# Optimization experiments

Hardware: AMD Instinct MI355X
Metric: run time of the kernel (lower is better)

The kernel has to match this reference:

```python
import jax, jax.numpy as jnp
import numpy as np

IRREPS = [0, 1, 2, 3, 4]   # l values; dim = sum(2l+1) = 25
MAX_L = max(IRREPS)
DIM = sum(2 * l + 1 for l in IRREPS)
EPS = 1e-14
N_POINTS = 200000


def _p_terms(i, a, b, l):
    """Ivanic-Ruedenberg P(i,l,a,b) as sparse terms: (coef, flat idx into R1 (3x3), flat idx into D^{l-1})."""
    lp = l - 1
    n = 2 * lp + 1
    row = i + 1  # R1 rows/cols indexed by m in {-1,0,1} -> {0,1,2}
    if b == l:
        return [(1.0, row * 3 + 2, (a + lp) * n + 2 * lp),
                (-1.0, row * 3 + 0, (a + lp) * n + 0)]
    if b == -l:
        return [(1.0, row * 3 + 2, (a + lp) * n + 0),
                (1.0, row * 3 + 0, (a + lp) * n + 2 * lp)]
    return [(1.0, row * 3 + 1, (a + lp) * n + (b + lp))]


def _ru_tables(l):
    """Precompute sparse recurrence tables for building D^l from D^{l-1} and R1."""
    out_idx, rij, ab, coef = [], [], [], []
    n = 2 * l + 1
    for m in range(-l, l + 1):
        for mp in range(-l, l + 1):
            denom = (2 * l) * (2 * l - 1) if abs(mp) == l else (l + mp) * (l - mp)
            d0 = 1.0 if m == 0 else 0.0
            u = np.sqrt((l + m) * (l - m) / denom)
            v = 0.5 * np.sqrt((1 + d0) * (l + abs(m) - 1) * (l + abs(m)) / denom) * (1 - 2 * d0)
            w = -0.5 * np.sqrt(max(l - abs(m) - 1, 0) * (l - abs(m)) / denom) * (1 - d0)
            terms = []
            if u != 0.0:
                terms += [(u * c, i, j) for c, i, j in _p_terms(0, m, mp, l)]
            if v != 0.0:
                if m == 0:
                    terms += [(v * c, i, j) for c, i, j in _p_terms(1, 1, mp, l)]
                    terms += [(v * c, i, j) for c, i, j in _p_terms(-1, -1, mp, l)]
                elif m > 0:
                    s = np.sqrt(2.0) if m == 1 else 1.0
                    terms += [(v * s * c, i, j) for c, i, j in _p_terms(1, m - 1, mp, l)]
                    if m != 1:
                        terms += [(-v * c, i, j) for c, i, j in _p_terms(-1, -m + 1, mp, l)]
                else:
                    if m != -1:
                        terms += [(v * c, i, j) for c, i, j in _p_terms(1, m + 1, mp, l)]
                    s = np.sqrt(2.0) if m == -1 else 1.0
                    terms += [(v * s * c, i, j) for c, i, j in _p_terms(-1, -m - 1, mp, l)]
            if w != 0.0:
                if m > 0:
                    terms += [(w * c, i, j) for c, i, j in _p_terms(1, m + 1, mp, l)]
                    terms += [(w * c, i, j) for c, i, j in _p_terms(-1, -m - 1, mp, l)]
                else:
                    terms += [(w * c, i, j) for c, i, j in _p_terms(1, m - 1, mp, l)]
                    terms += [(-w * c, i, j) for c, i, j in _p_terms(-1, -m + 1, mp, l)]
            o = (m + l) * n + (mp + l)
            for c, i, j in terms:
                out_idx.append(o); rij.append(i); ab.append(j); coef.append(c)
    return (np.asarray(out_idx), np.asarray(rij), np.asarray(ab),
            np.asarray(coef, dtype=np.float32))


_TABLES = {l: _ru_tables(l) for l in range(2, MAX_L + 1)}


def _wigner_blocks(R1, max_l):
    """D^l for real spherical harmonics via Ivanic-Ruedenberg recurrence. R1: (N,3,3)."""
    N = R1.shape[0]
    blocks = {0: jnp.ones((N, 1, 1), R1.dtype), 1: R1}
    r1f = R1.reshape(N, 9)
    for l in range(2, max_l + 1):
        oi, rij, ab, cf = _TABLES[l]
        dprev = blocks[l - 1].reshape(N, (2 * l - 1) ** 2)
        contrib = cf[None, :] * r1f[:, rij] * dprev[:, ab]  # (N, n_terms)
        n = 2 * l + 1
        Dl = jnp.zeros((N, n * n), R1.dtype).at[:, oi].add(contrib)
        blocks[l] = Dl.reshape(N, n, n)
    return blocks


def _forward(xyz):
    # angles of v (normalized=True): theta polar, phi azimuthal
    norm = jnp.linalg.norm(xyz, axis=-1, keepdims=True)
    v = xyz / jnp.maximum(norm, EPS)
    ct = jnp.clip(v[..., 2], -1.0, 1.0)
    theta = jnp.arccos(ct)
    phi = jnp.arctan2(v[..., 1], v[..., 0])
    st, cp, sp = jnp.sin(theta), jnp.cos(phi), jnp.sin(phi)
    z = jnp.zeros_like(ct)
    # R = Ry(-theta) @ Rz(-phi): R @ v = |v| z_hat
    R = jnp.stack([
        jnp.stack([ct * cp, ct * sp, -st], -1),
        jnp.stack([-sp, cp, z], -1),
        jnp.stack([st * cp, st * sp, ct], -1),
    ], -2)  # (N,3,3)
    # real-SH l=1 basis order m=(-1,0,1) <-> (y,z,x)
    p = jnp.array([1, 2, 0])
    R1 = R[:, p][:, :, p]
    blocks = _wigner_blocks(R1, MAX_L)
    N = xyz.shape[0]
    D = jnp.zeros((N, DIM, DIM), xyz.dtype)
    off = 0
    for l in IRREPS:
        d = 2 * l + 1
        D = D.at[:, off:off + d, off:off + d].set(blocks[l])
        off += d
    return D


def setup_inputs() -> dict:
    key = jax.random.key(0)
    xyz = jax.random.normal(key, (N_POINTS, 3), dtype=jnp.float32)
    return {"xyz": xyz}


def reference(xyz):
    return _forward(xyz)
```

## Files before the change

kernel.cpp:

```cpp
#include <hip/hip_runtime.h>
#include <utility>
#include <cstddef>


struct Term { int o; int r; int a; float c; };
struct LTable { int n; Term t[1024]; };

constexpr double csqrt(double x) {
    if (x <= 0.0) return 0.0;
    double g = x < 1.0 ? 1.0 : x;
    for (int i = 0; i < 50; ++i) g = 0.5 * (g + x / g);
    return g;
}
constexpr int cabs_i(int x) { return x < 0 ? -x : x; }
constexpr int cmax_i(int a, int b) { return a > b ? a : b; }

constexpr void add_p(LTable& T, int o, double scale, int i, int a, int b, int l) {
    int lp = l - 1;
    int np = 2 * lp + 1;
    int row = i + 1;
    if (b == l) {
        T.t[T.n++] = Term{o, row * 3 + 2, (a + lp) * np + 2 * lp, (float)scale};
        T.t[T.n++] = Term{o, row * 3 + 0, (a + lp) * np + 0,      (float)(-scale)};
    } else if (b == -l) {
        T.t[T.n++] = Term{o, row * 3 + 2, (a + lp) * np + 0,      (float)scale};
        T.t[T.n++] = Term{o, row * 3 + 0, (a + lp) * np + 2 * lp, (float)scale};
    } else {
        T.t[T.n++] = Term{o, row * 3 + 1, (a + lp) * np + (b + lp), (float)scale};
    }
}

constexpr LTable ru_table(int l) {
    LTable T{};
    int n = 2 * l + 1;
    for (int m = -l; m <= l; ++m) {
        for (int mp = -l; mp <= l; ++mp) {
            double denom = (cabs_i(mp) == l) ? (double)((2 * l) * (2 * l - 1))
                                             : (double)((l + mp) * (l - mp));
            double d0 = (m == 0) ? 1.0 : 0.0;
            double u = csqrt((double)((l + m) * (l - m)) / denom);
            double v = 0.5 * csqrt((1.0 + d0) * (l + cabs_i(m) - 1) * (l + cabs_i(m)) / denom)
                       * (1.0 - 2.0 * d0);
            double w = -0.5 * csqrt((double)cmax_i(l - cabs_i(m) - 1, 0) * (l - cabs_i(m)) / denom)
                       * (1.0 - d0);
            int o = (m + l) * n + (mp + l);
            if (u != 0.0) add_p(T, o, u, 0, m, mp, l);
            if (v != 0.0) {
                if (m == 0) {
                    add_p(T, o, v, 1, 1, mp, l);
                    add_p(T, o, v, -1, -1, mp, l);
                } else if (m > 0) {
                    double s = (m == 1) ? csqrt(2.0) : 1.0;
                    add_p(T, o, v * s, 1, m - 1, mp, l);
                    if (m != 1) add_p(T, o, -v, -1, -m + 1, mp, l);
                } else {
                    if (m != -1) add_p(T, o, v, 1, m + 1, mp, l);
                    double s = (m == -1) ? csqrt(2.0) : 1.0;
                    add_p(T, o, v * s, -1, -m - 1, mp, l);
                }
            }
            if (w != 0.0) {
                if (m > 0) {
                    add_p(T, o, w, 1, m + 1, mp, l);
                    add_p(T, o, w, -1, -m - 1, mp, l);
                } else {
                    add_p(T, o, w, 1, m - 1, mp, l);
                    add_p(T, o, -w, -1, -m + 1, mp, l);
                }
            }
        }
    }
    return T;
}

inline constexpr LTable T2 = ru_table(2);
inline constexpr LTable T3 = ru_table(3);
inline constexpr LTable T4 = ru_table(4);

template<const LTable& T>
constexpr int er_start(int e) {
    for (int i = 0; i < T.n; ++i) if (T.t[i].o == e) return i;
    return 0;
}
template<const LTable& T>
constexpr int er_cnt(int e) {
    int c = 0;
    for (int i = 0; i < T.n; ++i) if (T.t[i].o == e) ++c;
    return c;
}

template<const LTable& T, int S, size_t... K>
__device__ __forceinline__ float sum_terms(const float* __restrict__ R1,
                                           const float* __restrict__ P,
                                           std::index_sequence<K...>) {
    float a = 0.0f;
    ((a = fmaf(T.t[S + (int)K].c, R1[T.t[S + (int)K].r] * P[T.t[S + (int)K].a], a)), ...);
    return a;
}

template<const LTable& T, int l, bool KEEP, int e>
__device__ __forceinline__ void level_one(const float* __restrict__ R1,
                                          const float* __restrict__ P,
                                          float* __restrict__ keep,
                                          float* __restrict__ row) {
    constexpr int S = er_start<T>(e);
    constexpr int C = er_cnt<T>(e);
    float v = sum_terms<T, S>(R1, P, std::make_index_sequence<C>{});
    if constexpr (KEEP) keep[e] = v;
    constexpr int d = 2 * l + 1;
    constexpr int r = e / d, c = e % d;
    constexpr int E625 = (l * l + r) * 25 + (l * l + c);
    row[E625] = v;
}

template<const LTable& T, int l, bool KEEP, size_t... E>
__device__ __forceinline__ void level(const float* __restrict__ R1,
                                      const float* __restrict__ P,
                                      float* __restrict__ keep,
                                      float* __restrict__ row,
                                      std::index_sequence<E...>) {
    (level_one<T, l, KEEP, (int)E>(R1, P, keep, row), ...);
}

template<size_t... E>
__device__ __forceinline__ void write_l1(const float* __restrict__ D1,
                                         float* __restrict__ row,
                                         std::index_sequence<E...>) {
    ((row[(1 + (int)E / 3) * 25 + (1 + (int)E % 3)] = D1[E]), ...);
}

typedef float v4f __attribute__((ext_vector_type(4)));


__global__ __launch_bounds__(256, 2)
void wigner_fused_kernel(const float* __restrict__ xyz, float* __restrict__ out, int Ntot) {
    __shared__ float img[32 * 625];

    const int t = threadIdx.x;
    const int gp = blockIdx.x * 256 + t;

    float x = 0.0f, y = 0.0f, z = 1.0f;
    if (gp < Ntot) {
        x = xyz[3 * gp + 0];
        y = xyz[3 * gp + 1];
        z = xyz[3 * gp + 2];
    }

    const float r2 = x * x + y * y + z * z;
    const float rinv = rsqrtf(fmaxf(r2, 1e-24f));
    const float ct = fminf(fmaxf(z * rinv, -1.0f), 1.0f);
    const float st = sqrtf(fmaxf(1.0f - ct * ct, 0.0f));
    const float rxy2 = x * x + y * y;
    float cp = 1.0f, sp = 0.0f;
    if (rxy2 > 0.0f) {
        const float ri = rsqrtf(rxy2);
        cp = x * ri;
        sp = y * ri;
    }

    v4f* b4 = (v4f*)img;
    const v4f z4 = {0.0f, 0.0f, 0.0f, 0.0f};
#pragma unroll 4
    for (int k = t; k < 5000; k += 256) b4[k] = z4;
    __syncthreads();

    const int p0 = t & 31;
    const long long blk_f = (long long)blockIdx.x * 256 * 625;

    for (int c = 0; c < 8; ++c) {
        const int base_pt = blockIdx.x * 256 + c * 32;
        if (base_pt >= Ntot) break;
        const int vp = min(32, Ntot - base_pt);

        if ((t >> 5) == c && gp < Ntot) {
            float* __restrict__ row = img + p0 * 625;
            row[0] = 1.0f;

            float D1[9] = {cp,      0.0f, -sp,
                           st * sp, ct,   st * cp,
                           ct * sp, -st,  ct * cp};
            write_l1(D1, row, std::make_index_sequence<9>{});

            float D2[25];
            level<T2, 2, true>(D1, D1, D2, row, std::make_index_sequence<25>{});
            float D3[49];
            level<T3, 3, true>(D1, D2, D3, row, std::make_index_sequence<49>{});
            level<T4, 4, false>(D1, D3, nullptr, row, std::make_index_sequence<81>{});
        }
        __syncthreads();

        const long long out_f = blk_f + (long long)c * 32 * 625;
        if (vp == 32) {
            const v4f* src = (const v4f*)img;
            v4f* dst = (v4f*)(out + out_f);
#pragma unroll 4
            for (int k = t; k < 5000; k += 256) {
                __builtin_nontemporal_store(src[k], dst + k);
            }
        } else {
            const int vf = vp * 625;
            for (int k = t; k < vf; k += 256) {
                out[out_f + k] = img[k];
            }
        }
        __syncthreads();
    }
}

extern "C" void kernel_launch(void* const* d_in, const int* in_sizes, int n_in,
                              void* d_out, int out_size, void* d_ws, size_t ws_size,
                              hipStream_t stream) {
    const float* xyz = (const float*)d_in[0];
    float* out = (float*)d_out;
    const int N = in_sizes[0] / 3;
    const int blocks = (N + 255) / 256;
    hipLaunchKernelGGL(wigner_fused_kernel, dim3(blocks), dim3(256), 0, stream,
                       xyz, out, N);
}
```

Before: 538.7 us.

## Split per-point Wigner recurrence across all eight warps via shared-memory levels

```diff
diff --git a/kernel.cpp b/kernel.cpp
--- a/kernel.cpp
+++ b/kernel.cpp
@@ -89,42 +89,61 @@
     return c;
 }
 
-template<const LTable& T, int S, size_t... K>
-__device__ __forceinline__ float sum_terms(const float* __restrict__ R1,
-                                           const float* __restrict__ P,
+constexpr int poff(int a, int l) {
+    int lp = l - 1;
+    int n = 2 * lp + 1;
+    int rr = a / n, cc = a % n;
+    return (lp * lp + rr) * 25 + (lp * lp + cc);
+}
+
+template<const LTable& T, int S, bool PREG, int l, int K>
+__device__ __forceinline__ float term_val(const float* R1, const float* P) {
+    constexpr Term tm = T.t[S + K];
+    constexpr int idx = PREG ? tm.a : poff(tm.a, l);
+    return R1[tm.r] * P[idx];
+}
+
+template<const LTable& T, int S, bool PREG, int l, size_t... K>
+__device__ __forceinline__ float sum_terms(const float* R1, const float* P,
                                            std::index_sequence<K...>) {
     float a = 0.0f;
-    ((a = fmaf(T.t[S + (int)K].c, R1[T.t[S + (int)K].r] * P[T.t[S + (int)K].a], a)), ...);
+    ((a = fmaf(T.t[S + (int)K].c, term_val<T, S, PREG, l, (int)K>(R1, P), a)), ...);
     return a;
 }
 
-template<const LTable& T, int l, bool KEEP, int e>
-__device__ __forceinline__ void level_one(const float* __restrict__ R1,
-                                          const float* __restrict__ P,
-                                          float* __restrict__ keep,
-                                          float* __restrict__ row) {
+template<const LTable& T, int l, bool PREG, int e>
+__device__ __forceinline__ void entry_one(const float* R1, const float* P,
+                                          float* row) {
     constexpr int S = er_start<T>(e);
     constexpr int C = er_cnt<T>(e);
-    float v = sum_terms<T, S>(R1, P, std::make_index_sequence<C>{});
-    if constexpr (KEEP) keep[e] = v;
+    float v = sum_terms<T, S, PREG, l>(R1, P, std::make_index_sequence<C>{});
     constexpr int d = 2 * l + 1;
-    constexpr int r = e / d, c = e % d;
-    constexpr int E625 = (l * l + r) * 25 + (l * l + c);
-    row[E625] = v;
-}
-
-template<const LTable& T, int l, bool KEEP, size_t... E>
-__device__ __forceinline__ void level(const float* __restrict__ R1,
-                                      const float* __restrict__ P,
-                                      float* __restrict__ keep,
-                                      float* __restrict__ row,
-                                      std::index_sequence<E...>) {
-    (level_one<T, l, KEEP, (int)E>(R1, P, keep, row), ...);
+    constexpr int off = (l * l + e / d) * 25 + (l * l + e % d);
+    row[off] = v;
+}
+
+template<const LTable& T, int l, bool PREG, int G, size_t... K>
+__device__ __forceinline__ void group_entries(const float* R1, const float* P,
+                                              float* row, std::index_sequence<K...>) {
+    (entry_one<T, l, PREG, G + 8 * (int)K>(R1, P, row), ...);
+}
+
+template<const LTable& T, int l, bool PREG>
+__device__ __forceinline__ void group_dispatch(int g, const float* R1,
+                                               const float* P, float* row) {
+    constexpr int NE = (2 * l + 1) * (2 * l + 1);
+    if      (g == 0) group_entries<T, l, PREG, 0>(R1, P, row, std::make_index_sequence<(NE - 0 + 7) / 8>{});
+    else if (g == 1) group_entries<T, l, PREG, 1>(R1, P, row, std::make_index_sequence<(NE - 1 + 7) / 8>{});
+    else if (g == 2) group_entries<T, l, PREG, 2>(R1, P, row, std::make_index_sequence<(NE - 2 + 7) / 8>{});
+    else if (g == 3) group_entries<T, l, PREG, 3>(R1, P, row, std::make_index_sequence<(NE - 3 + 7) / 8>{});
+    else if (g == 4) group_entries<T, l, PREG, 4>(R1, P, row, std::make_index_sequence<(NE - 4 + 7) / 8>{});
+    else if (g == 5) group_entries<T, l, PREG, 5>(R1, P, row, std::make_index_sequence<(NE - 5 + 7) / 8>{});
+    else if (g == 6) group_entries<T, l, PREG, 6>(R1, P, row, std::make_index_sequence<(NE - 6 + 7) / 8>{});
+    else             group_entries<T, l, PREG, 7>(R1, P, row, std::make_index_sequence<(NE - 7 + 7) / 8>{});
 }
 
 template<size_t... E>
-__device__ __forceinline__ void write_l1(const float* __restrict__ D1,
-                                         float* __restrict__ row,
+__device__ __forceinline__ void write_l1(const float* D1, float* row,
                                          std::index_sequence<E...>) {
     ((row[(1 + (int)E / 3) * 25 + (1 + (int)E % 3)] = D1[E]), ...);
 }
@@ -137,26 +156,8 @@
     __shared__ float img[32 * 625];
 
     const int t = threadIdx.x;
-    const int gp = blockIdx.x * 256 + t;
-
-    float x = 0.0f, y = 0.0f, z = 1.0f;
-    if (gp < Ntot) {
-        x = xyz[3 * gp + 0];
-        y = xyz[3 * gp + 1];
-        z = xyz[3 * gp + 2];
-    }
-
-    const float r2 = x * x + y * y + z * z;
-    const float rinv = rsqrtf(fmaxf(r2, 1e-24f));
-    const float ct = fminf(fmaxf(z * rinv, -1.0f), 1.0f);
-    const float st = sqrtf(fmaxf(1.0f - ct * ct, 0.0f));
-    const float rxy2 = x * x + y * y;
-    float cp = 1.0f, sp = 0.0f;
-    if (rxy2 > 0.0f) {
-        const float ri = rsqrtf(rxy2);
-        cp = x * ri;
-        sp = y * ri;
-    }
+    const int p = t & 31;
+    const int g = t >> 5;
 
     v4f* b4 = (v4f*)img;
     const v4f z4 = {0.0f, 0.0f, 0.0f, 0.0f};
@@ -164,29 +165,51 @@
     for (int k = t; k < 5000; k += 256) b4[k] = z4;
     __syncthreads();
 
-    const int p0 = t & 31;
     const long long blk_f = (long long)blockIdx.x * 256 * 625;
+    float* row = img + p * 625;
 
     for (int c = 0; c < 8; ++c) {
         const int base_pt = blockIdx.x * 256 + c * 32;
         if (base_pt >= Ntot) break;
         const int vp = min(32, Ntot - base_pt);
-
-        if ((t >> 5) == c && gp < Ntot) {
-            float* __restrict__ row = img + p0 * 625;
-            row[0] = 1.0f;
-
-            float D1[9] = {cp,      0.0f, -sp,
-                           st * sp, ct,   st * cp,
-                           ct * sp, -st,  ct * cp};
-            write_l1(D1, row, std::make_index_sequence<9>{});
-
-            float D2[25];
-            level<T2, 2, true>(D1, D1, D2, row, std::make_index_sequence<25>{});
-            float D3[49];
-            level<T3, 3, true>(D1, D2, D3, row, std::make_index_sequence<49>{});
-            level<T4, 4, false>(D1, D3, nullptr, row, std::make_index_sequence<81>{});
-        }
+        const int pt = base_pt + p;
+        const bool live = (p < vp);
+
+        float x = 0.0f, y = 0.0f, z = 1.0f;
+        if (live) {
+            x = xyz[3 * pt + 0];
+            y = xyz[3 * pt + 1];
+            z = xyz[3 * pt + 2];
+        }
+        const float r2 = x * x + y * y + z * z;
+        const float rinv = rsqrtf(fmaxf(r2, 1e-24f));
+        const float ct = fminf(fmaxf(z * rinv, -1.0f), 1.0f);
+        const float st = sqrtf(fmaxf(1.0f - ct * ct, 0.0f));
+        const float rxy2 = x * x + y * y;
+        float cp = 1.0f, sp = 0.0f;
+        if (rxy2 > 0.0f) {
+            const float ri = rsqrtf(rxy2);
+            cp = x * ri;
+            sp = y * ri;
+        }
+
+        const float R1[9] = {cp,      0.0f, -sp,
+                             st * sp, ct,   st * cp,
+                             ct * sp, -st,  ct * cp};
+
+        if (live) {
+            if (g == 0) {
+                row[0] = 1.0f;
+                write_l1(R1, row, std::make_index_sequence<9>{});
+            }
+            group_dispatch<T2, 2, true>(g, R1, R1, row);
+        }
+        __syncthreads();
+
+        if (live) group_dispatch<T3, 3, false>(g, R1, row, row);
+        __syncthreads();
+
+        if (live) group_dispatch<T4, 4, false>(g, R1, row, row);
         __syncthreads();
 
         const long long out_f = blk_f + (long long)c * 32 * 625;
```

After: 560.9 us. 1.04x slower.

## Compute Wigner entries per wave and stream 64-column slices through LDS transpose

Applied to the files above, without the earlier changes.

```diff
diff --git a/kernel.cpp b/kernel.cpp
--- a/kernel.cpp
+++ b/kernel.cpp
@@ -98,52 +98,112 @@
     return a;
 }
 
-template<const LTable& T, int l, bool KEEP, int e>
-__device__ __forceinline__ void level_one(const float* __restrict__ R1,
+template<const LTable& T, size_t... E>
+__device__ __forceinline__ void level_reg(const float* __restrict__ R1,
                                           const float* __restrict__ P,
-                                          float* __restrict__ keep,
-                                          float* __restrict__ row) {
-    constexpr int S = er_start<T>(e);
-    constexpr int C = er_cnt<T>(e);
-    float v = sum_terms<T, S>(R1, P, std::make_index_sequence<C>{});
-    if constexpr (KEEP) keep[e] = v;
-    constexpr int d = 2 * l + 1;
-    constexpr int r = e / d, c = e % d;
-    constexpr int E625 = (l * l + r) * 25 + (l * l + c);
-    row[E625] = v;
-}
-
-template<const LTable& T, int l, bool KEEP, size_t... E>
-__device__ __forceinline__ void level(const float* __restrict__ R1,
-                                      const float* __restrict__ P,
-                                      float* __restrict__ keep,
-                                      float* __restrict__ row,
-                                      std::index_sequence<E...>) {
-    (level_one<T, l, KEEP, (int)E>(R1, P, keep, row), ...);
-}
-
-template<size_t... E>
-__device__ __forceinline__ void write_l1(const float* __restrict__ D1,
-                                         float* __restrict__ row,
-                                         std::index_sequence<E...>) {
-    ((row[(1 + (int)E / 3) * 25 + (1 + (int)E % 3)] = D1[E]), ...);
+                                          float* __restrict__ D,
+                                          std::index_sequence<E...>) {
+    ((D[(int)E] = sum_terms<T, er_start<T>((int)E)>(
+          R1, P, std::make_index_sequence<er_cnt<T>((int)E)>{})), ...);
+}
+
+
+constexpr int lof(int R) { return R >= 16 ? 4 : R >= 9 ? 3 : R >= 4 ? 2 : R >= 1 ? 1 : 0; }
+
+template<int f>
+__device__ __forceinline__ float entry_val(const float* __restrict__ R1,
+                                           const float* __restrict__ D2,
+                                           const float* __restrict__ D3) {
+    constexpr int R = f / 25, C = f % 25;
+    constexpr int lR = lof(R), lC = lof(C);
+    if constexpr (lR != lC) {
+        return 0.0f;
+    } else if constexpr (lR == 0) {
+        return 1.0f;
+    } else if constexpr (lR == 1) {
+        return R1[(R - 1) * 3 + (C - 1)];
+    } else if constexpr (lR == 2) {
+        return D2[(R - 4) * 5 + (C - 4)];
+    } else if constexpr (lR == 3) {
+        return D3[(R - 9) * 7 + (C - 9)];
+    } else {
+        constexpr int e = (R - 16) * 9 + (C - 16);
+        constexpr int S4 = er_start<T4>(e);
+        constexpr int C4 = er_cnt<T4>(e);
+        return sum_terms<T4, S4>(R1, D3, std::make_index_sequence<C4>{});
+    }
 }
 
 typedef float v4f __attribute__((ext_vector_type(4)));
+
+template<int S, int K>
+__device__ __forceinline__ v4f make_chunk(const float* __restrict__ R1,
+                                          const float* __restrict__ D2,
+                                          const float* __restrict__ D3) {
+    v4f v;
+    v.x = entry_val<S + 4 * K + 0>(R1, D2, D3);
+    v.y = entry_val<S + 4 * K + 1>(R1, D2, D3);
+    v.z = entry_val<S + 4 * K + 2>(R1, D2, D3);
+    v.w = entry_val<S + 4 * K + 3>(R1, D2, D3);
+    return v;
+}
+
+template<int S, size_t... K>
+__device__ __forceinline__ void write_slice(v4f* __restrict__ vrow,
+                                            const float* __restrict__ R1,
+                                            const float* __restrict__ D2,
+                                            const float* __restrict__ D3,
+                                            std::index_sequence<K...>) {
+    ((vrow[(int)K] = make_chunk<S, (int)K>(R1, D2, D3)), ...);
+}
+
+template<int S>
+__device__ __forceinline__ void emit_slice(v4f* __restrict__ vrow,
+                                           const float* __restrict__ strip,
+                                           float* __restrict__ obase,
+                                           long long wbase, int lane, int Ntot,
+                                           bool full,
+                                           const float* __restrict__ R1,
+                                           const float* __restrict__ D2,
+                                           const float* __restrict__ D3) {
+    write_slice<S>(vrow, R1, D2, D3, std::make_index_sequence<16>{});
+    asm volatile("s_waitcnt lgkmcnt(0)" ::: "memory");
+    if (full) {
+#pragma unroll
+        for (int j = 0; j < 64; ++j) {
+            __builtin_nontemporal_store(strip[68 * j + lane], obase + S + 625 * j);
+        }
+    } else {
+#pragma unroll 1
+        for (int j = 0; j < 64; ++j) {
+            if (wbase + j < Ntot) {
+                __builtin_nontemporal_store(strip[68 * j + lane], obase + S + 625 * j);
+            }
+        }
+    }
+    asm volatile("" ::: "memory");
+}
 
 
 __global__ __launch_bounds__(256, 2)
 void wigner_fused_kernel(const float* __restrict__ xyz, float* __restrict__ out, int Ntot) {
-    __shared__ float img[32 * 625];
+    __shared__ __align__(16) float lds[4 * 64 * 68];
 
     const int t = threadIdx.x;
-    const int gp = blockIdx.x * 256 + t;
+    const int w = t >> 6;
+    const int lane = t & 63;
+    float* __restrict__ strip = lds + w * (64 * 68);
+
+    const long long wbase = (long long)blockIdx.x * 256 + (long long)w * 64;
+    if (wbase >= Ntot) return;
+    const long long pt = wbase + lane;
+    const bool full = (wbase + 64 <= (long long)Ntot);
 
     float x = 0.0f, y = 0.0f, z = 1.0f;
-    if (gp < Ntot) {
-        x = xyz[3 * gp + 0];
-        y = xyz[3 * gp + 1];
-        z = xyz[3 * gp + 2];
+    if (pt < Ntot) {
+        x = xyz[3 * pt + 0];
+        y = xyz[3 * pt + 1];
+        z = xyz[3 * pt + 2];
     }
 
     const float r2 = x * x + y * y + z * z;
@@ -158,53 +218,28 @@
         sp = y * ri;
     }
 
-    v4f* b4 = (v4f*)img;
-    const v4f z4 = {0.0f, 0.0f, 0.0f, 0.0f};
-#pragma unroll 4
-    for (int k = t; k < 5000; k += 256) b4[k] = z4;
-    __syncthreads();
-
-    const int p0 = t & 31;
-    const long long blk_f = (long long)blockIdx.x * 256 * 625;
-
-    for (int c = 0; c < 8; ++c) {
-        const int base_pt = blockIdx.x * 256 + c * 32;
-        if (base_pt >= Ntot) break;
-        const int vp = min(32, Ntot - base_pt);
-
-        if ((t >> 5) == c && gp < Ntot) {
-            float* __restrict__ row = img + p0 * 625;
-            row[0] = 1.0f;
-
-            float D1[9] = {cp,      0.0f, -sp,
-                           st * sp, ct,   st * cp,
-                           ct * sp, -st,  ct * cp};
-            write_l1(D1, row, std::make_index_sequence<9>{});
-
-            float D2[25];
-            level<T2, 2, true>(D1, D1, D2, row, std::make_index_sequence<25>{});
-            float D3[49];
-            level<T3, 3, true>(D1, D2, D3, row, std::make_index_sequence<49>{});
-            level<T4, 4, false>(D1, D3, nullptr, row, std::make_index_sequence<81>{});
-        }
-        __syncthreads();
-
-        const long long out_f = blk_f + (long long)c * 32 * 625;
-        if (vp == 32) {
-            const v4f* src = (const v4f*)img;
-            v4f* dst = (v4f*)(out + out_f);
-#pragma unroll 4
-            for (int k = t; k < 5000; k += 256) {
-                __builtin_nontemporal_store(src[k], dst + k);
-            }
-        } else {
-            const int vf = vp * 625;
-            for (int k = t; k < vf; k += 256) {
-                out[out_f + k] = img[k];
-            }
-        }
-        __syncthreads();
-    }
+    const float R1[9] = {cp,      0.0f, -sp,
+                         st * sp, ct,   st * cp,
+                         ct * sp, -st,  ct * cp};
+
+    float D2[25];
+    level_reg<T2>(R1, R1, D2, std::make_index_sequence<25>{});
+    float D3[49];
+    level_reg<T3>(R1, D2, D3, std::make_index_sequence<49>{});
+
+    v4f* __restrict__ vrow = (v4f*)(strip + 68 * lane);
+    float* __restrict__ obase = out + wbase * 625 + lane;
+
+    emit_slice<0  >(vrow, strip, obase, wbase, lane, Ntot, full, R1, D2, D3);
+    emit_slice<64 >(vrow, strip, obase, wbase, lane, Ntot, full, R1, D2, D3);
+    emit_slice<128>(vrow, strip, obase, wbase, lane, Ntot, full, R1, D2, D3);
+    emit_slice<192>(vrow, strip, obase, wbase, lane, Ntot, full, R1, D2, D3);
+    emit_slice<256>(vrow, strip, obase, wbase, lane, Ntot, full, R1, D2, D3);
+    emit_slice<320>(vrow, strip, obase, wbase, lane, Ntot, full, R1, D2, D3);
+    emit_slice<384>(vrow, strip, obase, wbase, lane, Ntot, full, R1, D2, D3);
+    emit_slice<448>(vrow, strip, obase, wbase, lane, Ntot, full, R1, D2, D3);
+    emit_slice<512>(vrow, strip, obase, wbase, lane, Ntot, full, R1, D2, D3);
+    emit_slice<561>(vrow, strip, obase, wbase, lane, Ntot, full, R1, D2, D3);
 }
 
 extern "C" void kernel_launch(void* const* d_in, const int* in_sizes, int n_in,
```

Measured after the change: 693.4 us. 1.29x slower.

## Compute all Wigner blocks in registers and stage output per-wavefront without block barriers

Applied to the files above, without the earlier changes.

```diff
diff --git a/kernel.cpp b/kernel.cpp
--- a/kernel.cpp
+++ b/kernel.cpp
@@ -98,35 +98,21 @@
     return a;
 }
 
-template<const LTable& T, int l, bool KEEP, int e>
-__device__ __forceinline__ void level_one(const float* __restrict__ R1,
+template<const LTable& T, size_t... E>
+__device__ __forceinline__ void level_reg(const float* __restrict__ R1,
                                           const float* __restrict__ P,
-                                          float* __restrict__ keep,
-                                          float* __restrict__ row) {
-    constexpr int S = er_start<T>(e);
-    constexpr int C = er_cnt<T>(e);
-    float v = sum_terms<T, S>(R1, P, std::make_index_sequence<C>{});
-    if constexpr (KEEP) keep[e] = v;
-    constexpr int d = 2 * l + 1;
-    constexpr int r = e / d, c = e % d;
-    constexpr int E625 = (l * l + r) * 25 + (l * l + c);
-    row[E625] = v;
-}
-
-template<const LTable& T, int l, bool KEEP, size_t... E>
-__device__ __forceinline__ void level(const float* __restrict__ R1,
-                                      const float* __restrict__ P,
-                                      float* __restrict__ keep,
-                                      float* __restrict__ row,
-                                      std::index_sequence<E...>) {
-    (level_one<T, l, KEEP, (int)E>(R1, P, keep, row), ...);
-}
-
-template<size_t... E>
-__device__ __forceinline__ void write_l1(const float* __restrict__ D1,
-                                         float* __restrict__ row,
-                                         std::index_sequence<E...>) {
-    ((row[(1 + (int)E / 3) * 25 + (1 + (int)E % 3)] = D1[E]), ...);
+                                          float* __restrict__ D,
+                                          std::index_sequence<E...>) {
+    ((D[(int)E] = sum_terms<T, er_start<T>((int)E)>(
+          R1, P, std::make_index_sequence<er_cnt<T>((int)E)>{})), ...);
+}
+
+template<int l, size_t... E>
+__device__ __forceinline__ void dump_level(const float* __restrict__ D,
+                                           float* __restrict__ row,
+                                           std::index_sequence<E...>) {
+    ((row[(l * l + (int)E / (2 * l + 1)) * 25 + (l * l + (int)E % (2 * l + 1))]
+          = D[(int)E]), ...);
 }
 
 typedef float v4f __attribute__((ext_vector_type(4)));
@@ -134,16 +120,22 @@
 
 __global__ __launch_bounds__(256, 2)
 void wigner_fused_kernel(const float* __restrict__ xyz, float* __restrict__ out, int Ntot) {
-    __shared__ float img[32 * 625];
+    __shared__ __align__(16) float lds[4][8 * 625];
 
     const int t = threadIdx.x;
-    const int gp = blockIdx.x * 256 + t;
+    const int w = t >> 6;
+    const int lane = t & 63;
+    float* __restrict__ strip = lds[w];
+
+    const long long wbase = (long long)blockIdx.x * 256 + (long long)w * 64;
+    if (wbase >= Ntot) return;
+    const long long pt = wbase + lane;
 
     float x = 0.0f, y = 0.0f, z = 1.0f;
-    if (gp < Ntot) {
-        x = xyz[3 * gp + 0];
-        y = xyz[3 * gp + 1];
-        z = xyz[3 * gp + 2];
+    if (pt < Ntot) {
+        x = xyz[3 * pt + 0];
+        y = xyz[3 * pt + 1];
+        z = xyz[3 * pt + 2];
     }
 
     const float r2 = x * x + y * y + z * z;
@@ -158,52 +150,52 @@
         sp = y * ri;
     }
 
-    v4f* b4 = (v4f*)img;
-    const v4f z4 = {0.0f, 0.0f, 0.0f, 0.0f};
+    const float R1[9] = {cp,      0.0f, -sp,
+                         st * sp, ct,   st * cp,
+                         ct * sp, -st,  ct * cp};
+
+    float D2[25];
+    level_reg<T2>(R1, R1, D2, std::make_index_sequence<25>{});
+    float D3[49];
+    level_reg<T3>(R1, D2, D3, std::make_index_sequence<49>{});
+    float D4[81];
+    level_reg<T4>(R1, D3, D4, std::make_index_sequence<81>{});
+
+    {
+        v4f* b4 = (v4f*)strip;
+        const v4f z4 = {0.0f, 0.0f, 0.0f, 0.0f};
 #pragma unroll 4
-    for (int k = t; k < 5000; k += 256) b4[k] = z4;
-    __syncthreads();
-
-    const int p0 = t & 31;
-    const long long blk_f = (long long)blockIdx.x * 256 * 625;
-
-    for (int c = 0; c < 8; ++c) {
-        const int base_pt = blockIdx.x * 256 + c * 32;
-        if (base_pt >= Ntot) break;
-        const int vp = min(32, Ntot - base_pt);
-
-        if ((t >> 5) == c && gp < Ntot) {
-            float* __restrict__ row = img + p0 * 625;
+        for (int k = lane; k < 1250; k += 64) b4[k] = z4;
+    }
+    asm volatile("s_waitcnt lgkmcnt(0)" ::: "memory");
+
+#pragma unroll 1
+    for (int r = 0; r < 8; ++r) {
+        const long long rbase = wbase + (long long)r * 8;
+        if (rbase >= Ntot) break;
+
+        if ((lane >> 3) == r && pt < Ntot) {
+            float* __restrict__ row = strip + (lane & 7) * 625;
             row[0] = 1.0f;
-
-            float D1[9] = {cp,      0.0f, -sp,
-                           st * sp, ct,   st * cp,
-                           ct * sp, -st,  ct * cp};
-            write_l1(D1, row, std::make_index_sequence<9>{});
-
-            float D2[25];
-            level<T2, 2, true>(D1, D1, D2, row, std::make_index_sequence<25>{});
-            float D3[49];
-            level<T3, 3, true>(D1, D2, D3, row, std::make_index_sequence<49>{});
-            level<T4, 4, false>(D1, D3, nullptr, row, std::make_index_sequence<81>{});
+            dump_level<1>(R1, row, std::make_index_sequence<9>{});
+            dump_level<2>(D2, row, std::make_index_sequence<25>{});
+            dump_level<3>(D3, row, std::make_index_sequence<49>{});
+            dump_level<4>(D4, row, std::make_index_sequence<81>{});
         }
-        __syncthreads();
-
-        const long long out_f = blk_f + (long long)c * 32 * 625;
-        if (vp == 32) {
-            const v4f* src = (const v4f*)img;
-            v4f* dst = (v4f*)(out + out_f);
+        asm volatile("s_waitcnt lgkmcnt(0)" ::: "memory");
+
+        const int valid = (int)(Ntot - rbase < 8 ? Ntot - rbase : 8);
+        if (valid == 8) {
+            const v4f* __restrict__ src = (const v4f*)strip;
+            v4f* __restrict__ dst = (v4f*)(out + rbase * 625);
 #pragma unroll 4
-            for (int k = t; k < 5000; k += 256) {
-                __builtin_nontemporal_store(src[k], dst + k);
-            }
+            for (int k = lane; k < 1250; k += 64) dst[k] = src[k];
         } else {
-            const int vf = vp * 625;
-            for (int k = t; k < vf; k += 256) {
-                out[out_f + k] = img[k];
-            }
+            const int vf = valid * 625;
+            float* __restrict__ dstf = out + rbase * 625;
+            for (int k = lane; k < vf; k += 64) dstf[k] = strip[k];
         }
-        __syncthreads();
+        asm volatile("s_waitcnt lgkmcnt(0)" ::: "memory");
     }
 }
 
```

Result: slower. 613.8 us (+14.0%).
